# Performance work log

Measured on AMD Instinct MI355X. Metric: run time of the kernel, lower is better.

## Reference

```python
import jax, jax.numpy as jnp
import numpy as np

NPOINT, RADIUS, NSAMPLE = 1024, 0.2, 32


def _fps(xyz, npoint):
    # xyz: (B, N, 3) -> (B, npoint) int32, iterative furthest point sampling
    B, N, _ = xyz.shape

    def step(carry, _):
        dists, far = carry  # (B,N), (B,)
        centroid = jnp.take_along_axis(xyz, far[:, None, None], axis=1)  # (B,1,3)
        d = jnp.sum((xyz - centroid) ** 2, axis=-1)  # (B,N)
        dists = jnp.minimum(dists, d)
        nxt = jnp.argmax(dists, axis=-1).astype(jnp.int32)
        return (dists, nxt), far

    init = (jnp.full((B, N), 1e10, xyz.dtype), jnp.zeros((B,), jnp.int32))
    _, idx = jax.lax.scan(step, init, None, length=npoint)
    return jnp.transpose(idx)  # (B, npoint)


def _ball_query(radius, nsample, xyz, new_xyz):
    # xyz: (B,N,3), new_xyz: (B,S,3) -> (B,S,nsample) int32
    N = xyz.shape[1]
    d2 = jnp.sum((new_xyz[:, :, None, :] - xyz[:, None, :, :]) ** 2, axis=-1)  # (B,S,N)
    # first-nsample-in-range semantics of PointNet++ ball_query
    key = jnp.where(d2 < radius * radius, jnp.arange(N, dtype=jnp.int32), N)
    neg, order = jax.lax.top_k(-key, nsample)  # smallest keys first
    valid = (-neg) < N
    return jnp.where(valid, order, order[..., :1])  # pad with first valid idx


def _group(feat, idx):
    # feat: (B,D,N), idx: (B,S,ns) -> (B,D,S,ns)
    return jax.vmap(lambda f, i: f[:, i])(feat, idx)


def _conv(x, w, b):
    # 1x1 Conv2d: x (B,C,S,ns), w (O,C), b (O)
    return jnp.einsum('oc,bcps->bops', w, x) + b[None, :, None, None]


def _bn(x, s, t):
    # inference BatchNorm folded into per-channel affine
    return x * s[None, :, None, None] + t[None, :, None, None]


def setup_inputs() -> dict:
    key = jax.random.key(0)
    ks = jax.random.split(key, 40)
    B, N, D = 16, 8192, 64
    BCH = 8  # max(8, 64 // 8)

    def w(k, shape, scale=0.1):
        return jax.random.normal(k, shape, jnp.float32) * scale

    def bn(k, c):
        k1, k2 = jax.random.split(k)
        return (jax.random.uniform(k1, (c,), jnp.float32, 0.75, 1.25),
                0.1 * jax.random.normal(k2, (c,), jnp.float32))

    attn_s0, attn_t0 = bn(ks[2], BCH)
    attn_s1, attn_t1 = bn(ks[3], D)
    attn_s2, attn_t2 = bn(ks[4], D)
    mlp_s0, mlp_t0 = bn(ks[5], 64)
    mlp_s1, mlp_t1 = bn(ks[6], 64)
    eca_s, eca_t = bn(ks[7], 128)
    return {
        'xyz': jax.random.uniform(ks[0], (B, 3, N), jnp.float32),
        'points': jax.random.normal(ks[1], (B, D, N), jnp.float32),
        'attn_w0': w(ks[10], (BCH, 3)), 'attn_b0': w(ks[11], (BCH,)),
        'attn_s0': attn_s0, 'attn_t0': attn_t0,
        'attn_w1': w(ks[12], (D, BCH)), 'attn_b1': w(ks[13], (D,)),
        'attn_s1': attn_s1, 'attn_t1': attn_t1,
        'attn_w2': w(ks[14], (D, D)), 'attn_b2': w(ks[15], (D,)),
        'attn_s2': attn_s2, 'attn_t2': attn_t2,
        'mlp_w0': w(ks[16], (64, D)), 'mlp_b0': w(ks[17], (64,)),
        'mlp_s0': mlp_s0, 'mlp_t0': mlp_t0,
        'mlp_w1': w(ks[18], (64, 64)), 'mlp_b1': w(ks[19], (64,)),
        'mlp_s1': mlp_s1, 'mlp_t1': mlp_t1,
        'eca_k': w(ks[20], (3,), 0.5),
        'eca_w': w(ks[21], (128, 64)), 'eca_b': w(ks[22], (128,)),
        'eca_s': eca_s, 'eca_t': eca_t,
    }


def reference(xyz, points,
              attn_w0, attn_b0, attn_s0, attn_t0,
              attn_w1, attn_b1, attn_s1, attn_t1,
              attn_w2, attn_b2, attn_s2, attn_t2,
              mlp_w0, mlp_b0, mlp_s0, mlp_t0,
              mlp_w1, mlp_b1, mlp_s1, mlp_t1,
              eca_k, eca_w, eca_b, eca_s, eca_t):
    xyz_f = jnp.transpose(xyz, (0, 2, 1))  # (B,N,3)
    # 1. sampling + grouping
    fps_idx = _fps(xyz_f, NPOINT)  # (B,S)
    new_xyz = jax.vmap(lambda p, i: p[:, i])(xyz, fps_idx)  # (B,3,S)
    idx = _ball_query(RADIUS, NSAMPLE, xyz_f, jnp.transpose(new_xyz, (0, 2, 1)))
    grouped_xyz = _group(xyz, idx) - new_xyz[..., None]  # (B,3,S,ns)
    x = _group(points, idx)  # (B,D,S,ns)
    # 2. position-attention module
    pos = jax.nn.relu(_bn(_conv(grouped_xyz, attn_w0, attn_b0), attn_s0, attn_t0))
    pos = _bn(_conv(pos, attn_w1, attn_b1), attn_s1, attn_t1)
    x = x + pos
    x = _bn(_conv(x, attn_w2, attn_b2), attn_s2, attn_t2)
    # 3. shared MLP (conv-bn-relu over mlp[:-1])
    x = jax.nn.relu(_bn(_conv(x, mlp_w0, mlp_b0), mlp_s0, mlp_t0))
    x = jax.nn.relu(_bn(_conv(x, mlp_w1, mlp_b1), mlp_s1, mlp_t1))
    # 4. ECA channel attention + final 1x1 conv-bn
    y = jnp.mean(x, axis=(2, 3))  # (B,C)
    yp = jnp.pad(y, ((0, 0), (1, 1)))
    y = eca_k[0] * yp[:, :-2] + eca_k[1] * yp[:, 1:-1] + eca_k[2] * yp[:, 2:]
    x = x * jax.nn.sigmoid(y)[:, :, None, None]
    x = _bn(_conv(x, eca_w, eca_b), eca_s, eca_t)
    # 5. max-pool over neighborhood
    new_features = jnp.max(x, axis=-1)  # (B,128,S)
    return (new_xyz, new_features)
```

## Files before the change

kernel.cpp:

```cpp
#include <hip/hip_runtime.h>

typedef unsigned int   u32;
typedef unsigned long long u64;
typedef float pkf2 __attribute__((ext_vector_type(2)));

#define B_  16
#define N_  8192
#define S_  1024
#define NS_ 32
#define XS_ 68
#define NWORK_ 240
#define NCHUNK_ 4096
#define NFIN_ 512

__device__ __forceinline__ float nanguard(float v) {
  u32 x = __float_as_uint(v);
  if ((x & 0x7F80u) == 0x7F80u) x ^= 0x0080u;
  return __uint_as_float(x);
}

__device__ __forceinline__ float wave_max_nonneg(float v) {
  int x = __float_as_int(v);
#define DPP_STEP(ctrl) \
  x = __float_as_int(fmaxf(__int_as_float(x), \
      __int_as_float(__builtin_amdgcn_update_dpp(0, x, (ctrl), 0xf, 0xf, true))))
  DPP_STEP(0x111);
  DPP_STEP(0x112);
  DPP_STEP(0x114);
  DPP_STEP(0x118);
  DPP_STEP(0x142);
  DPP_STEP(0x143);
#undef DPP_STEP
  return __int_as_float(__builtin_amdgcn_readlane(x, 63));
}

__global__ __launch_bounds__(256) void k_xyzt(const float* __restrict__ xyz, float4* __restrict__ xyzt,
                                              u32* __restrict__ prog) {
  if (blockIdx.x == 0 && blockIdx.y == 0 && threadIdx.x < 16) prog[threadIdx.x] = 0u;
  int b = blockIdx.y;
  int i = blockIdx.x * 256 + threadIdx.x;
  const float* p = xyz + (size_t)b * 3 * N_;
  xyzt[(size_t)b * N_ + i] = make_float4(p[i], p[N_ + i], p[2 * N_ + i], 0.f);
}

__global__ __launch_bounds__(256) void k_ptst(const float* __restrict__ pts, float* __restrict__ ptst) {
  __shared__ float tile[64][65];
  int b = blockIdx.y, n0 = blockIdx.x * 64, t = threadIdx.x;
  {
    int c = t >> 2, j0 = (t & 3) * 16;
    const float4* src = (const float4*)(pts + (size_t)b * 64 * N_ + (size_t)c * N_ + n0 + j0);
#pragma unroll
    for (int q = 0; q < 4; ++q) {
      float4 a = src[q];
      tile[c][j0 + 4*q + 0] = a.x; tile[c][j0 + 4*q + 1] = a.y;
      tile[c][j0 + 4*q + 2] = a.z; tile[c][j0 + 4*q + 3] = a.w;
    }
  }
  __syncthreads();
  {
    int n = t >> 2, c0 = (t & 3) * 16;
    float4* dv = (float4*)(ptst + ((size_t)b * N_ + n0 + n) * 64 + c0);
#pragma unroll
    for (int q = 0; q < 4; ++q)
      dv[q] = make_float4(tile[c0 + 4*q + 0][n], tile[c0 + 4*q + 1][n],
                          tile[c0 + 4*q + 2][n], tile[c0 + 4*q + 3][n]);
  }
}

__global__ __launch_bounds__(1024)
__attribute__((amdgpu_waves_per_eu(4, 4)))
void k_fps(const float4* __restrict__ xyzt,
           float4* __restrict__ nxf,
           float* __restrict__ out_xyz) {
#pragma clang fp contract(off)
  __shared__ float4 ldsp[N_];
  __shared__ u64 slot[4];
  __shared__ int win_hist[S_];
  int b = blockIdx.x, t = threadIdx.x;
  const float4* p4 = xyzt + (size_t)b * N_;
  const float4* pp8 = p4 + t * 8;

  float4 q0 = pp8[0], q1 = pp8[1], q2 = pp8[2], q3 = pp8[3];
  float4 q4 = pp8[4], q5 = pp8[5], q6 = pp8[6], q7 = pp8[7];
  ldsp[t * 8 + 0] = q0; ldsp[t * 8 + 1] = q1; ldsp[t * 8 + 2] = q2; ldsp[t * 8 + 3] = q3;
  ldsp[t * 8 + 4] = q4; ldsp[t * 8 + 5] = q5; ldsp[t * 8 + 6] = q6; ldsp[t * 8 + 7] = q7;

#define DECLPAIR(P, A, B) \
  pkf2 px##P = {q##A.x, q##B.x}; pkf2 py##P = {q##A.y, q##B.y}; \
  pkf2 pz##P = {q##A.z, q##B.z}; pkf2 dm##P = {1e10f, 1e10f};
  DECLPAIR(01, 0, 1) DECLPAIR(23, 2, 3) DECLPAIR(45, 4, 5) DECLPAIR(67, 6, 7)
#undef DECLPAIR
#define PIN(P) asm volatile("" : "+v"(px##P), "+v"(py##P), "+v"(pz##P));
  PIN(01) PIN(23) PIN(45) PIN(67)
#undef PIN

  if (t == 0) {
    slot[0] = 8191ull;
    slot[1] = 0; slot[2] = 0; slot[3] = 0;
    win_hist[0] = 0;
  }
  __syncthreads();
  int lane = t & 63;
  for (int it = 1; it < S_; ++it) {
    u64 w = slot[(it - 1) & 3];
    int widx = 8191 - (int)(w & 0xFFFFFFFFull);
    if (t == 0) { win_hist[it - 1] = widx; slot[(it + 1) & 3] = 0; }
    float4 c = ldsp[widx & (N_ - 1)];
    pkf2 cx2 = {c.x, c.x}, cy2 = {c.y, c.y}, cz2 = {c.z, c.z};
#define UPDP(P) { \
    pkf2 dx = px##P - cx2; pkf2 dy = py##P - cy2; pkf2 dz = pz##P - cz2; \
    pkf2 xx = dx * dx; pkf2 yy = dy * dy; pkf2 zz = dz * dz; \
    pkf2 ss = xx + yy; pkf2 dd = ss + zz; \
    dm##P.x = fminf(dm##P.x, dd.x); dm##P.y = fminf(dm##P.y, dd.y); }
    UPDP(01) UPDP(23) UPDP(45) UPDP(67)
#undef UPDP
    float e0 = dm01.x, e1 = dm01.y, e2 = dm23.x, e3 = dm23.y;
    float e4 = dm45.x, e5 = dm45.y, e6 = dm67.x, e7 = dm67.y;
    float va0 = e1 > e0 ? e1 : e0; int ia0 = e1 > e0 ? 1 : 0;
    float va1 = e3 > e2 ? e3 : e2; int ia1 = e3 > e2 ? 3 : 2;
    float va2 = e5 > e4 ? e5 : e4; int ia2 = e5 > e4 ? 5 : 4;
    float va3 = e7 > e6 ? e7 : e6; int ia3 = e7 > e6 ? 7 : 6;
    float vb0 = va1 > va0 ? va1 : va0; int ib0 = va1 > va0 ? ia1 : ia0;
    float vb1 = va3 > va2 ? va3 : va2; int ib1 = va3 > va2 ? ia3 : ia2;
    float bv = vb1 > vb0 ? vb1 : vb0;  int bk = vb1 > vb0 ? ib1 : ib0;
    int bi = t * 8 + bk;
    float wm = wave_max_nonneg(bv);
    u64 msk = __ballot(bv == wm);
    int wl = __ffsll((long long)msk) - 1;
    int wbi = __builtin_amdgcn_readlane(bi, wl);
    if (lane == 0)
      atomicMax(&slot[it & 3],
                ((u64)__float_as_uint(wm) << 32) | (u64)(u32)(8191 - wbi));
    __syncthreads();
  }
  if (t == 0)
    win_hist[S_ - 1] = 8191 - (int)(slot[(S_ - 1) & 3] & 0xFFFFFFFFull);
  __syncthreads();
  {
    int wi = win_hist[t] & (N_ - 1);
    float4 c = ldsp[wi];
    nxf[(size_t)b * S_ + t] = c;
    float* o = out_xyz + (size_t)b * 3 * S_;
    o[t] = nanguard(c.x); o[S_ + t] = nanguard(c.y); o[2 * S_ + t] = nanguard(c.z);
  }
}

__global__ __launch_bounds__(256) void k_ball(const float4* __restrict__ xyzt,
                                              const float4* __restrict__ nxf,
                                              int* __restrict__ ballidx) {
  int gw = blockIdx.x * 4 + (threadIdx.x >> 6);
  int lane = threadIdx.x & 63;
  int b = gw >> 10, s = gw & 1023;
  float4 c = nxf[(size_t)b * S_ + s];
  const float4* pts = xyzt + (size_t)b * N_;
  int* out = ballidx + (size_t)gw * NS_;
  int cnt = 0, first = 0;
  bool havefirst = false;
  for (int chunk = 0; chunk < N_; chunk += 64) {
    float4 p = pts[chunk + lane];
    float dx = p.x - c.x, dy = p.y - c.y, dz = p.z - c.z;
    float d2 = __fadd_rn(__fadd_rn(__fmul_rn(dx, dx), __fmul_rn(dy, dy)), __fmul_rn(dz, dz));
    bool v = d2 <= 0.04f;
    u64 m = __ballot(v);
    if (m) {
      int pos = cnt + __popcll(m & ((1ull << lane) - 1ull));
      if (v && pos < NS_) out[pos] = chunk + lane;
      if (!havefirst) { first = chunk + (__ffsll((long long)m) - 1); havefirst = true; }
      cnt += __popcll(m);
      if (cnt >= NS_) break;
    }
  }
  if (cnt < NS_) {
    for (int p = cnt + lane; p < NS_; p += 64) out[p] = first;
  }
}

struct ChainSm {
  float Wbuf[64 * XS_];
  float W1f[64 * 9];
  float W0f[8 * 4];
  float s2f[64], sm0f[64], sm1f[64];
  float bb0[8];
  float bb1[64], bb2[64], bm0[64], bm1[64];
  float X[32 * XS_];
  float H[32 * XS_];
  float scratch[384];
  int   idx_s[NS_];
};

__device__ __forceinline__ void stage_w64(float* Wbuf, const float* w, int t) {
  int c = t >> 2, q = (t & 3) * 16;
  const float4* src = (const float4*)(w + c * 64 + q);
  float4* dst = (float4*)(Wbuf + c * XS_ + q);
  dst[0] = src[0]; dst[1] = src[1]; dst[2] = src[2]; dst[3] = src[3];
}

template<bool RELU>
__device__ __forceinline__ void gemm64(const float* __restrict__ Wbuf,
                                       const float* __restrict__ Xin,
                                       float* __restrict__ Yout,
                                       const float* __restrict__ scl,
                                       const float* __restrict__ bia,
                                       int lane, int n0) {
  float acc[8] = {0,0,0,0,0,0,0,0};
#pragma unroll
  for (int k4 = 0; k4 < 16; ++k4) {
    float4 wq = *(const float4*)&Wbuf[lane * XS_ + k4 * 4];
#pragma unroll
    for (int nj = 0; nj < 8; ++nj) {
      float4 xq = *(const float4*)&Xin[(n0 + nj) * XS_ + k4 * 4];
      acc[nj] += wq.x * xq.x; acc[nj] += wq.y * xq.y;
      acc[nj] += wq.z * xq.z; acc[nj] += wq.w * xq.w;
    }
  }
  float sc = scl[lane], bi = bia[lane];
#pragma unroll
  for (int nj = 0; nj < 8; ++nj) {
    float v = sc * acc[nj] + bi;
    Yout[(n0 + nj) * XS_ + lane] = RELU ? fmaxf(v, 0.f) : v;
  }
}

template<bool USE_PTST>
__device__ __forceinline__ void chain_tile(ChainSm& sm, int b, int s, int bs,
    const float4* xyzt, const float* ptst, const float* points,
    const float4* nxf, const int* ballidx,
    const float* w0, const float* b0, const float* s0, const float* t0,
    const float* w1, const float* b1, const float* s1, const float* t1,
    const float* w2, const float* b2, const float* s2, const float* t2,
    const float* m0w, const float* m0b, const float* m0s, const float* m0t,
    const float* m1w, const float* m1b, const float* m1s, const float* m1t) {
  int t = threadIdx.x, lane = t & 63, g = t >> 6, n0 = g * 8;

  stage_w64(sm.Wbuf, w2, t);
  if (t < 64) {
    float v2 = s2[t];  sm.s2f[t] = v2;  sm.bb2[t] = v2 * b2[t] + t2[t];
    float vm0 = m0s[t]; sm.sm0f[t] = vm0; sm.bm0[t] = vm0 * m0b[t] + m0t[t];
    float vm1 = m1s[t]; sm.sm1f[t] = vm1; sm.bm1[t] = vm1 * m1b[t] + m1t[t];
    float v1 = s1[t];
#pragma unroll
    for (int k = 0; k < 8; ++k) sm.W1f[t * 9 + k] = v1 * w1[t * 8 + k];
    sm.bb1[t] = v1 * b1[t] + t1[t];
  }
  if (t < 8) {
    float v0 = s0[t];
#pragma unroll
    for (int k = 0; k < 3; ++k) sm.W0f[t * 4 + k] = v0 * w0[t * 3 + k];
    sm.bb0[t] = v0 * b0[t] + t0[t];
  }
  if (t < NS_) sm.idx_s[t] = ballidx[(size_t)bs * NS_ + t] & (N_ - 1);
  __syncthreads();

  {
    int n = t >> 3, c8 = (t & 7) * 8;
    int pi = sm.idx_s[n];
    if (USE_PTST) {
      const float4* v = (const float4*)(ptst + ((size_t)b * N_ + pi) * 64 + c8);
      float4* xr = (float4*)&sm.X[n * XS_ + c8];
      xr[0] = v[0]; xr[1] = v[1];
    } else {
      const float* pp = points + (size_t)b * 64 * N_ + (size_t)c8 * N_ + pi;
#pragma unroll
      for (int j = 0; j < 8; ++j) sm.X[n * XS_ + c8 + j] = pp[(size_t)j * N_];
    }
  }
  if (t < NS_) {
    float4 p = xyzt[(size_t)b * N_ + sm.idx_s[t]];
    float4 cc = nxf[(size_t)b * S_ + s];
    float* gx = &sm.scratch[256 + t * 4];
    gx[0] = p.x - cc.x; gx[1] = p.y - cc.y; gx[2] = p.z - cc.z;
  }
  __syncthreads();

  {
    int n = t >> 3, cc = t & 7;
    const float* gx = &sm.scratch[256 + n * 4];
    float a = sm.bb0[cc];
    a += sm.W0f[cc * 4 + 0] * gx[0];
    a += sm.W0f[cc * 4 + 1] * gx[1];
    a += sm.W0f[cc * 4 + 2] * gx[2];
    sm.scratch[n * 8 + cc] = fmaxf(a, 0.f);
  }
  {
#pragma unroll
    for (int nj = 0; nj < 8; ++nj) {
      float a = sm.bb1[lane];
      const float* p8 = &sm.scratch[(n0 + nj) * 8];
#pragma unroll
      for (int k = 0; k < 8; ++k) a += sm.W1f[lane * 9 + k] * p8[k];
      sm.X[(n0 + nj) * XS_ + lane] += a;
    }
  }
  gemm64<false>(sm.Wbuf, sm.X, sm.H, sm.s2f, sm.bb2, lane, n0);
  __syncthreads();
  stage_w64(sm.Wbuf, m0w, t);
  __syncthreads();
  gemm64<true>(sm.Wbuf, sm.H, sm.X, sm.sm0f, sm.bm0, lane, n0);
  __syncthreads();
  stage_w64(sm.Wbuf, m1w, t);
  __syncthreads();
  gemm64<true>(sm.Wbuf, sm.X, sm.H, sm.sm1f, sm.bm1, lane, n0);
}

template<bool USE_PTST, bool WRITE_H2>
__global__ __launch_bounds__(256) void k_chain(
    const float4* __restrict__ xyzt, const float* __restrict__ ptst,
    const float* __restrict__ points,
    const float4* __restrict__ nxf, const int* __restrict__ ballidx,
    const float* w0, const float* b0, const float* s0, const float* t0,
    const float* w1, const float* b1, const float* s1, const float* t1,
    const float* w2, const float* b2, const float* s2, const float* t2,
    const float* m0w, const float* m0b, const float* m0s, const float* m0t,
    const float* m1w, const float* m1b, const float* m1s, const float* m1t,
    float* __restrict__ h2out, float* __restrict__ partials) {
  __shared__ ChainSm sm;
  int t = threadIdx.x, bs = blockIdx.x;
  int b = bs >> 10, s = bs & 1023;
  int lane = t & 63, g = t >> 6, n0 = g * 8;

  chain_tile<USE_PTST>(sm, b, s, bs, xyzt, ptst, points, nxf, ballidx,
                       w0, b0, s0, t0, w1, b1, s1, t1, w2, b2, s2, t2,
                       m0w, m0b, m0s, m0t, m1w, m1b, m1s, m1t);

  float* psum = sm.scratch;
  float lsum = 0.f;
#pragma unroll
  for (int nj = 0; nj < 8; ++nj) {
    float r = sm.H[(n0 + nj) * XS_ + lane];
    lsum += r;
    if (WRITE_H2)
      h2out[((size_t)bs * 32 + n0 + nj) * 64 + lane] = r;
  }
  psum[lane * 5 + g] = lsum;
  __syncthreads();
  if (t < 64) {
    float v = (psum[t * 5 + 0] + psum[t * 5 + 1]) + (psum[t * 5 + 2] + psum[t * 5 + 3]);
    partials[(size_t)bs * 64 + t] = v;
  }
}

struct ChainSub {
  float X[32 * XS_];
  float H[32 * XS_];
  float scratch[384];
  int   idx_s[NS_];
};
struct WkSm {
  float Wc2[64 * XS_];
  float Wm0[64 * XS_];
  float Wm1[64 * XS_];
  float W1f[64 * 9];
  float W0f[8 * 4];
  float s2f[64], sm0f[64], sm1f[64];
  float bb0[8];
  float bb1[64], bb2[64], bm0[64], bm1[64];
  ChainSub sub[4];
};
struct FpsSm {
  float4 ldsp[N_];
  u64 slot[4];
  int win_hist[S_];
};
union FusedSm { FpsSm f; WkSm w; };
static_assert(sizeof(FusedSm) <= 160 * 1024, "LDS overflow");

__global__ __launch_bounds__(1024)
__attribute__((amdgpu_waves_per_eu(4, 4)))
void k_fused(const float4* __restrict__ xyzt, const float* __restrict__ ptst,
             float4* __restrict__ nxf, float* __restrict__ out_xyz,
             u32* __restrict__ prog,
             const float* w0, const float* b0, const float* s0, const float* t0,
             const float* w1, const float* b1, const float* s1, const float* t1,
             const float* w2, const float* b2, const float* s2, const float* t2,
             const float* m0w, const float* m0b, const float* m0s, const float* m0t,
             const float* m1w, const float* m1b, const float* m1s, const float* m1t,
             float* __restrict__ h2out, float* __restrict__ partials) {
  __shared__ FusedSm smu;
  int t = threadIdx.x;

  if (blockIdx.x < B_) {
#pragma clang fp contract(off)
    FpsSm& fs = smu.f;
    int b = blockIdx.x;
    const float4* p4 = xyzt + (size_t)b * N_;
    const float4* pp8 = p4 + t * 8;

    float4 q0 = pp8[0], q1 = pp8[1], q2 = pp8[2], q3 = pp8[3];
    float4 q4 = pp8[4], q5 = pp8[5], q6 = pp8[6], q7 = pp8[7];
    fs.ldsp[t * 8 + 0] = q0; fs.ldsp[t * 8 + 1] = q1; fs.ldsp[t * 8 + 2] = q2; fs.ldsp[t * 8 + 3] = q3;
    fs.ldsp[t * 8 + 4] = q4; fs.ldsp[t * 8 + 5] = q5; fs.ldsp[t * 8 + 6] = q6; fs.ldsp[t * 8 + 7] = q7;

#define DECLPAIR(P, A, B) \
    pkf2 px##P = {q##A.x, q##B.x}; pkf2 py##P = {q##A.y, q##B.y}; \
    pkf2 pz##P = {q##A.z, q##B.z}; pkf2 dm##P = {1e10f, 1e10f};
    DECLPAIR(01, 0, 1) DECLPAIR(23, 2, 3) DECLPAIR(45, 4, 5) DECLPAIR(67, 6, 7)
#undef DECLPAIR
#define PIN(P) asm volatile("" : "+v"(px##P), "+v"(py##P), "+v"(pz##P));
    PIN(01) PIN(23) PIN(45) PIN(67)
#undef PIN

    if (t == 0) {
      fs.slot[0] = 8191ull;
      fs.slot[1] = 0; fs.slot[2] = 0; fs.slot[3] = 0;
      fs.win_hist[0] = 0;
    }
    __syncthreads();
    int lane = t & 63;
    for (int it = 1; it < S_; ++it) {
      u64 w = fs.slot[(it - 1) & 3];
      int widx = 8191 - (int)(w & 0xFFFFFFFFull);
      float4 c = fs.ldsp[widx & (N_ - 1)];
      if (t == 0) {
        fs.win_hist[it - 1] = widx; fs.slot[(it + 1) & 3] = 0;
        if ((it & 15) == 0)
          __hip_atomic_store(&prog[b], (u32)(it - 1), __ATOMIC_RELEASE, __HIP_MEMORY_SCOPE_AGENT);
        nxf[(size_t)b * S_ + (it - 1)] = c;
      }
      pkf2 cx2 = {c.x, c.x}, cy2 = {c.y, c.y}, cz2 = {c.z, c.z};
#define UPDP(P) { \
      pkf2 dx = px##P - cx2; pkf2 dy = py##P - cy2; pkf2 dz = pz##P - cz2; \
      pkf2 xx = dx * dx; pkf2 yy = dy * dy; pkf2 zz = dz * dz; \
      pkf2 ss = xx + yy; pkf2 dd = ss + zz; \
      dm##P.x = fminf(dm##P.x, dd.x); dm##P.y = fminf(dm##P.y, dd.y); }
      UPDP(01) UPDP(23) UPDP(45) UPDP(67)
#undef UPDP
      float e0 = dm01.x, e1 = dm01.y, e2 = dm23.x, e3 = dm23.y;
      float e4 = dm45.x, e5 = dm45.y, e6 = dm67.x, e7 = dm67.y;
      float va0 = e1 > e0 ? e1 : e0; int ia0 = e1 > e0 ? 1 : 0;
      float va1 = e3 > e2 ? e3 : e2; int ia1 = e3 > e2 ? 3 : 2;
      float va2 = e5 > e4 ? e5 : e4; int ia2 = e5 > e4 ? 5 : 4;
      float va3 = e7 > e6 ? e7 : e6; int ia3 = e7 > e6 ? 7 : 6;
      float vb0 = va1 > va0 ? va1 : va0; int ib0 = va1 > va0 ? ia1 : ia0;
      float vb1 = va3 > va2 ? va3 : va2; int ib1 = va3 > va2 ? ia3 : ia2;
      float bv = vb1 > vb0 ? vb1 : vb0;  int bk = vb1 > vb0 ? ib1 : ib0;
      int bi = t * 8 + bk;
      float wm = wave_max_nonneg(bv);
      u64 msk = __ballot(bv == wm);
      int wl = __ffsll((long long)msk) - 1;
      int wbi = __builtin_amdgcn_readlane(bi, wl);
      if (lane == 0)
        atomicMax(&fs.slot[it & 3],
                  ((u64)__float_as_uint(wm) << 32) | (u64)(u32)(8191 - wbi));
      __syncthreads();
    }
    if (t == 0) {
      int wl_ = 8191 - (int)(fs.slot[(S_ - 1) & 3] & 0xFFFFFFFFull);
      fs.win_hist[S_ - 1] = wl_;
      float4 c = fs.ldsp[wl_ & (N_ - 1)];
      nxf[(size_t)b * S_ + (S_ - 1)] = c;
    }
    __syncthreads();
    {
      int wi = fs.win_hist[t] & (N_ - 1);
      float4 c = fs.ldsp[wi];
      float* o = out_xyz + (size_t)b * 3 * S_;
      o[t] = nanguard(c.x); o[S_ + t] = nanguard(c.y); o[2 * S_ + t] = nanguard(c.z);
    }
    if (t == 0)
      __hip_atomic_store(&prog[b], (u32)S_, __ATOMIC_RELEASE, __HIP_MEMORY_SCOPE_AGENT);
    return;
  }

  WkSm& wk = smu.w;
  int w = blockIdx.x - B_;
  if (t < 256) {
    stage_w64(wk.Wc2, w2, t);
    stage_w64(wk.Wm0, m0w, t);
    stage_w64(wk.Wm1, m1w, t);
  }
  if (t < 64) {
    float v2 = s2[t];  wk.s2f[t] = v2;  wk.bb2[t] = v2 * b2[t] + t2[t];
    float vm0 = m0s[t]; wk.sm0f[t] = vm0; wk.bm0[t] = vm0 * m0b[t] + m0t[t];
    float vm1 = m1s[t]; wk.sm1f[t] = vm1; wk.bm1[t] = vm1 * m1b[t] + m1t[t];
    float v1 = s1[t];
#pragma unroll
    for (int k = 0; k < 8; ++k) wk.W1f[t * 9 + k] = v1 * w1[t * 8 + k];
    wk.bb1[t] = v1 * b1[t] + t1[t];
  }
  if (t < 8) {
    float v0 = s0[t];
#pragma unroll
    for (int k = 0; k < 3; ++k) wk.W0f[t * 4 + k] = v0 * w0[t * 3 + k];
    wk.bb0[t] = v0 * b0[t] + t0[t];
  }
  __syncthreads();

  int sg = t >> 8, tid = t & 255, lane = t & 63, g2 = (t >> 6) & 3, n0 = g2 * 8;
  ChainSub& cs = wk.sub[sg];

  for (int ck = w; ck < NCHUNK_; ck += NWORK_) {
    int s = ck >> 2, bg = ck & 3, b = bg * 4 + sg;
    if (t == 0) {
      int bbase = bg * 4;
#pragma unroll
      for (int j = 0; j < 4; ++j) {
        while (__hip_atomic_load(&prog[bbase + j], __ATOMIC_RELAXED, __HIP_MEMORY_SCOPE_AGENT) < (u32)(s + 1))
          __builtin_amdgcn_s_sleep(32);
      }
      (void)__hip_atomic_load(&prog[bbase], __ATOMIC_ACQUIRE, __HIP_MEMORY_SCOPE_AGENT);
    }
    __syncthreads();

    float4 cc;
    if (g2 == 0) {
      cc = nxf[(size_t)b * S_ + s];
      const float4* pts = xyzt + (size_t)b * N_;
      int cnt = 0, first = 0;
      bool havefirst = false;
      for (int chunk = 0; chunk < N_; chunk += 64) {
        float4 p = pts[chunk + lane];
        float dx = p.x - cc.x, dy = p.y - cc.y, dz = p.z - cc.z;
        float d2 = __fadd_rn(__fadd_rn(__fmul_rn(dx, dx), __fmul_rn(dy, dy)), __fmul_rn(dz, dz));
        bool v = d2 <= 0.04f;
        u64 m = __ballot(v);
        if (m) {
          int pos = cnt + __popcll(m & ((1ull << lane) - 1ull));
          if (v && pos < NS_) cs.idx_s[pos] = chunk + lane;
          if (!havefirst) { first = chunk + (__ffsll((long long)m) - 1); havefirst = true; }
          cnt += __popcll(m);
          if (cnt >= NS_) break;
        }
      }
      if (cnt < NS_) {
        for (int p = cnt + lane; p < NS_; p += 64) cs.idx_s[p] = first;
      }
    }
    __syncthreads();

    {
      int n = tid >> 3, c8 = (tid & 7) * 8;
      int pi = cs.idx_s[n];
      const float4* v = (const float4*)(ptst + ((size_t)b * N_ + pi) * 64 + c8);
      float4* xr = (float4*)&cs.X[n * XS_ + c8];
      xr[0] = v[0]; xr[1] = v[1];
    }
    if (tid < NS_) {
      float4 p = xyzt[(size_t)b * N_ + cs.idx_s[tid]];
      float* gx = &cs.scratch[256 + tid * 4];
      gx[0] = p.x - cc.x; gx[1] = p.y - cc.y; gx[2] = p.z - cc.z;
    }
    __syncthreads();

    {
      int n = tid >> 3, ch = tid & 7;
      const float* gx = &cs.scratch[256 + n * 4];
      float a = wk.bb0[ch];
      a += wk.W0f[ch * 4 + 0] * gx[0];
      a += wk.W0f[ch * 4 + 1] * gx[1];
      a += wk.W0f[ch * 4 + 2] * gx[2];
      cs.scratch[n * 8 + ch] = fmaxf(a, 0.f);
    }
    {
#pragma unroll
      for (int nj = 0; nj < 8; ++nj) {
        float a = wk.bb1[lane];
        const float* p8 = &cs.scratch[(n0 + nj) * 8];
#pragma unroll
        for (int k = 0; k < 8; ++k) a += wk.W1f[lane * 9 + k] * p8[k];
        cs.X[(n0 + nj) * XS_ + lane] += a;
      }
    }
    gemm64<false>(wk.Wc2, cs.X, cs.H, wk.s2f, wk.bb2, lane, n0);
    gemm64<true >(wk.Wm0, cs.H, cs.X, wk.sm0f, wk.bm0, lane, n0);
    gemm64<true >(wk.Wm1, cs.X, cs.H, wk.sm1f, wk.bm1, lane, n0);

    int bs = (b << 10) | s;
    float lsum = 0.f;
#pragma unroll
    for (int nj = 0; nj < 8; ++nj) {
      float r = cs.H[(n0 + nj) * XS_ + lane];
      lsum += r;
      h2out[((size_t)bs * 32 + n0 + nj) * 64 + lane] = r;
    }
    __syncthreads();
    cs.scratch[lane * 5 + g2] = lsum;
    __syncthreads();
    if (tid < 64) {
      float v = (cs.scratch[tid * 5 + 0] + cs.scratch[tid * 5 + 1]) +
                (cs.scratch[tid * 5 + 2] + cs.scratch[tid * 5 + 3]);
      partials[(size_t)bs * 64 + tid] = v;
    }
  }
}

__global__ __launch_bounds__(256) void k_eca(const float* __restrict__ partials,
                                             const float* __restrict__ ecak,
                                             float* __restrict__ sig) {
  __shared__ float red[64 * 5];
  __shared__ float yy[66];
  int b = blockIdx.x, t = threadIdx.x;
  int c = t & 63, sg = t >> 6;
  float acc = 0.f;
  for (int s = sg; s < S_; s += 4) acc += partials[((size_t)b * S_ + s) * 64 + c];
  red[c * 5 + sg] = acc;
  __syncthreads();
  if (t < 64) {
    float v = (red[t * 5 + 0] + red[t * 5 + 1]) + (red[t * 5 + 2] + red[t * 5 + 3]);
    yy[t + 1] = v * (1.f / 32768.f);
  }
  if (t == 64) { yy[0] = 0.f; yy[65] = 0.f; }
  __syncthreads();
  if (t < 64) {
    float gv = ecak[0] * yy[t] + ecak[1] * yy[t + 1] + ecak[2] * yy[t + 2];
    sig[b * 64 + t] = 1.f / (1.f + expf(-gv));
  }
}

__global__ __launch_bounds__(256, 2) void k_final_h2(const float* __restrict__ h2,
                                                     const float* __restrict__ sig,
                                                     const float* ew, const float* eb,
                                                     const float* es, const float* et,
                                                     float* __restrict__ outf) {
  __shared__ float Wh[128 * XS_];
  __shared__ float esf[128], bbf[128];
  __shared__ float X2[4][32 * XS_];
  int t = threadIdx.x;
  {
    int c2 = t >> 1, h = (t & 1) * 32;
    const float4* src = (const float4*)(ew + c2 * 64 + h);
    float4* dst = (float4*)(Wh + c2 * XS_ + h);
#pragma unroll
    for (int j = 0; j < 8; ++j) dst[j] = src[j];
  }
  if (t < 128) { float v = es[t]; esf[t] = v; bbf[t] = v * eb[t] + et[t]; }
  __syncthreads();

  int wv = t >> 6, lane = t & 63;
  int cg = lane & 15, rg = lane >> 4;
  float* X = X2[wv];
  int gw = blockIdx.x * 4 + wv;

  for (int bs = gw; bs < B_ * S_; bs += NFIN_ * 4) {
    int b = bs >> 10, s = bs & 1023;
    {
      float4 sgl = *(const float4*)&sig[b * 64 + cg * 4];
      const float4* hsrc = (const float4*)(h2 + (size_t)bs * 2048);
#pragma unroll
      for (int m = 0; m < 8; ++m) {
        int q = lane + 64 * m;
        float4 v = hsrc[q];
        v.x *= sgl.x; v.y *= sgl.y; v.z *= sgl.z; v.w *= sgl.w;
        *(float4*)&X[(q >> 4) * XS_ + (q & 15) * 4] = v;
      }
    }
#pragma unroll
    for (int half = 0; half < 2; ++half) {
      float acc[4][8];
#pragma unroll
      for (int i = 0; i < 4; ++i)
#pragma unroll
        for (int j = 0; j < 8; ++j) acc[i][j] = 0.f;
#pragma unroll
      for (int k4 = 0; k4 < 16; ++k4) {
        float4 xq[8];
#pragma unroll
        for (int j = 0; j < 8; ++j)
          xq[j] = *(const float4*)&X[(rg + 4 * j) * XS_ + k4 * 4];
#pragma unroll
        for (int i = 0; i < 4; ++i) {
          float4 wq = *(const float4*)&Wh[(half * 64 + cg + 16 * i) * XS_ + k4 * 4];
#pragma unroll
          for (int j = 0; j < 8; ++j) {
            acc[i][j] += wq.x * xq[j].x; acc[i][j] += wq.y * xq[j].y;
            acc[i][j] += wq.z * xq[j].z; acc[i][j] += wq.w * xq[j].w;
          }
        }
      }
      float m0, m1, m2, m3;
#define RED(i, mv) { \
      float a0 = fmaxf(fmaxf(acc[i][0], acc[i][1]), fmaxf(acc[i][2], acc[i][3])); \
      float a1 = fmaxf(fmaxf(acc[i][4], acc[i][5]), fmaxf(acc[i][6], acc[i][7])); \
      mv = fmaxf(a0, a1); \
      mv = fmaxf(mv, __shfl_xor(mv, 16)); \
      mv = fmaxf(mv, __shfl_xor(mv, 32)); }
      RED(0, m0) RED(1, m1) RED(2, m2) RED(3, m3)
#undef RED
      float msel = rg == 0 ? m0 : rg == 1 ? m1 : rg == 2 ? m2 : m3;
      int c = half * 64 + cg + 16 * rg;
      outf[((size_t)b * 128 + c) * S_ + s] = nanguard(esf[c] * msel + bbf[c]);
    }
  }
}

__device__ __forceinline__ void final_gemm(const float* __restrict__ WA,
                                           const float* __restrict__ WB,
                                           const float* __restrict__ X2,
                                           const float* __restrict__ esf,
                                           const float* __restrict__ bbf,
                                           float* __restrict__ zred,
                                           float* __restrict__ outf,
                                           int b, int s, int t) {
  int lane = t & 63, g = t >> 6, n0 = g * 8;
  float aA[8] = {0,0,0,0,0,0,0,0}, aB[8] = {0,0,0,0,0,0,0,0};
#pragma unroll
  for (int k4 = 0; k4 < 16; ++k4) {
    float4 wqA = *(const float4*)&WA[lane * XS_ + k4 * 4];
    float4 wqB = *(const float4*)&WB[lane * XS_ + k4 * 4];
#pragma unroll
    for (int nj = 0; nj < 8; ++nj) {
      float4 xq = *(const float4*)&X2[(n0 + nj) * XS_ + k4 * 4];
      aA[nj] += wqA.x * xq.x; aA[nj] += wqA.y * xq.y;
      aA[nj] += wqA.z * xq.z; aA[nj] += wqA.w * xq.w;
      aB[nj] += wqB.x * xq.x; aB[nj] += wqB.y * xq.y;
      aB[nj] += wqB.z * xq.z; aB[nj] += wqB.w * xq.w;
    }
  }
  float mA = aA[0], mB = aB[0];
#pragma unroll
  for (int j = 1; j < 8; ++j) { mA = fmaxf(mA, aA[j]); mB = fmaxf(mB, aB[j]); }
  zred[lane * 5 + g]        = esf[lane] * mA + bbf[lane];
  zred[(lane + 64) * 5 + g] = esf[lane + 64] * mB + bbf[lane + 64];
  __syncthreads();
  if (t < 128) {
    float m = fmaxf(fmaxf(zred[t * 5 + 0], zred[t * 5 + 1]),
                    fmaxf(zred[t * 5 + 2], zred[t * 5 + 3]));
    outf[((size_t)b * 128 + t) * S_ + s] = nanguard(m);
  }
}

template<bool USE_PTST>
__global__ __launch_bounds__(256) void k_final_rec(
    const float4* __restrict__ xyzt, const float* __restrict__ ptst,
    const float* __restrict__ points,
    const float4* __restrict__ nxf, const int* __restrict__ ballidx,
    const float* w0, const float* b0, const float* s0, const float* t0,
    const float* w1, const float* b1, const float* s1, const float* t1,
    const float* w2, const float* b2, const float* s2, const float* t2,
    const float* m0w, const float* m0b, const float* m0s, const float* m0t,
    const float* m1w, const float* m1b, const float* m1s, const float* m1t,
    const float* __restrict__ sig,
    const float* ew, const float* eb, const float* es, const float* et,
    float* __restrict__ outf) {
  __shared__ ChainSm sm;
  __shared__ float Wb2[64 * XS_];
  __shared__ float esf2[128], bbf2[128], sigl2[64];
  __shared__ float zred[128 * 5];
  int t = threadIdx.x, bs = blockIdx.x;
  int b = bs >> 10, s = bs & 1023;
  int lane = t & 63, g = t >> 6, n0 = g * 8;

  chain_tile<USE_PTST>(sm, b, s, bs, xyzt, ptst, points, nxf, ballidx,
                       w0, b0, s0, t0, w1, b1, s1, t1, w2, b2, s2, t2,
                       m0w, m0b, m0s, m0t, m1w, m1b, m1s, m1t);

  __syncthreads();
  stage_w64(sm.Wbuf, ew, t);
  stage_w64(Wb2, ew + 64 * 64, t);
  if (t < 128) {
    float v = es[t]; esf2[t] = v; bbf2[t] = v * eb[t] + et[t];
  }
  if (t < 64) sigl2[t] = sig[b * 64 + t];
  __syncthreads();
  {
#pragma unroll
    for (int nj = 0; nj < 8; ++nj)
      sm.X[(n0 + nj) * XS_ + lane] = sigl2[lane] * sm.H[(n0 + nj) * XS_ + lane];
  }
  final_gemm(sm.Wbuf, Wb2, sm.X, esf2, bbf2, zred, outf, b, s, t);
}

extern "C" void kernel_launch(void* const* d_in, const int* in_sizes, int n_in,
                              void* d_out, int out_size, void* d_ws, size_t ws_size,
                              hipStream_t stream) {
  const float* xyz    = (const float*)d_in[0];
  const float* points = (const float*)d_in[1];
  const float* w0 = (const float*)d_in[2],  *b0 = (const float*)d_in[3],  *s0 = (const float*)d_in[4],  *t0 = (const float*)d_in[5];
  const float* w1 = (const float*)d_in[6],  *b1 = (const float*)d_in[7],  *s1 = (const float*)d_in[8],  *t1 = (const float*)d_in[9];
  const float* w2 = (const float*)d_in[10], *b2 = (const float*)d_in[11], *s2 = (const float*)d_in[12], *t2 = (const float*)d_in[13];
  const float* m0w = (const float*)d_in[14], *m0b = (const float*)d_in[15], *m0s = (const float*)d_in[16], *m0t = (const float*)d_in[17];
  const float* m1w = (const float*)d_in[18], *m1b = (const float*)d_in[19], *m1s = (const float*)d_in[20], *m1t = (const float*)d_in[21];
  const float* ecak = (const float*)d_in[22];
  const float* ew = (const float*)d_in[23], *eb = (const float*)d_in[24], *es = (const float*)d_in[25], *et = (const float*)d_in[26];

  const size_t OFF_XYZT = 0;
  const size_t OFF_NXF  = 2097152;
  const size_t OFF_BIDX = 2359296;
  const size_t OFF_PART = 4456448;
  const size_t OFF_SIG  = 8650752;
  const size_t OFF_PTST = 8654848;
  const size_t OFF_H2   = 42209280;
  const size_t NEED_PTST = OFF_H2;
  const size_t NEED_H2   = 176427008;

  const bool use_ptst = ws_size >= NEED_PTST;
  const bool use_h2   = ws_size >= NEED_H2;

  char* ws = (char*)d_ws;
  float4* xyzt    = (float4*)(ws + OFF_XYZT);
  float4* nxf     = (float4*)(ws + OFF_NXF);
  int*    ballidx = (int*)   (ws + OFF_BIDX);
  u32*    prog    = (u32*)   (ws + OFF_BIDX);
  float*  partials= (float*) (ws + OFF_PART);
  float*  sig     = (float*) (ws + OFF_SIG);
  float*  ptst    = (float*) (ws + OFF_PTST);
  float*  h2      = (float*) (ws + OFF_H2);

  float* out_xyz  = (float*)d_out;
  float* out_feat = (float*)d_out + (size_t)B_ * 3 * S_;

  k_xyzt<<<dim3(N_ / 256, B_), 256, 0, stream>>>(xyz, xyzt, prog);
  if (use_ptst)
    k_ptst<<<dim3(N_ / 64, B_), 256, 0, stream>>>(points, ptst);

  if (use_h2) {
    k_fused<<<B_ + NWORK_, 1024, 0, stream>>>(xyzt, ptst, nxf, out_xyz, prog,
        w0, b0, s0, t0, w1, b1, s1, t1, w2, b2, s2, t2,
        m0w, m0b, m0s, m0t, m1w, m1b, m1s, m1t, h2, partials);
    k_eca<<<B_, 256, 0, stream>>>(partials, ecak, sig);
    k_final_h2<<<NFIN_, 256, 0, stream>>>(h2, sig, ew, eb, es, et, out_feat);
  } else if (use_ptst) {
    k_fps <<<B_, 1024, 0, stream>>>(xyzt, nxf, out_xyz);
    k_ball<<<(B_ * S_) / 4, 256, 0, stream>>>(xyzt, nxf, ballidx);
    k_chain<true, false><<<B_ * S_, 256, 0, stream>>>(xyzt, ptst, points, nxf, ballidx,
        w0, b0, s0, t0, w1, b1, s1, t1, w2, b2, s2, t2,
        m0w, m0b, m0s, m0t, m1w, m1b, m1s, m1t, h2, partials);
    k_eca<<<B_, 256, 0, stream>>>(partials, ecak, sig);
    k_final_rec<true><<<B_ * S_, 256, 0, stream>>>(xyzt, ptst, points, nxf, ballidx,
        w0, b0, s0, t0, w1, b1, s1, t1, w2, b2, s2, t2,
        m0w, m0b, m0s, m0t, m1w, m1b, m1s, m1t, sig, ew, eb, es, et, out_feat);
  } else {
    k_fps <<<B_, 1024, 0, stream>>>(xyzt, nxf, out_xyz);
    k_ball<<<(B_ * S_) / 4, 256, 0, stream>>>(xyzt, nxf, ballidx);
    k_chain<false, false><<<B_ * S_, 256, 0, stream>>>(xyzt, ptst, points, nxf, ballidx,
        w0, b0, s0, t0, w1, b1, s1, t1, w2, b2, s2, t2,
        m0w, m0b, m0s, m0t, m1w, m1b, m1s, m1t, h2, partials);
    k_eca<<<B_, 256, 0, stream>>>(partials, ecak, sig);
    k_final_rec<false><<<B_ * S_, 256, 0, stream>>>(xyzt, ptst, points, nxf, ballidx,
        w0, b0, s0, t0, w1, b1, s1, t1, w2, b2, s2, t2,
        m0w, m0b, m0s, m0t, m1w, m1b, m1s, m1t, sig, ew, eb, es, et, out_feat);
  }
}
```

Measured before the change: 1.245 ms.

## Fold ECA and final conv into fused persistent kernel via grid-wide counters

Removes the separate ECA and final conv/max-pool launches by running both inside the persistent fused kernel. Global atomic counters act as grid barriers: the FPS blocks wait for all worker blocks, compute the per-batch sigmoid gate, then signal, and every block then runs its slice of the final GEMM and max-pool. The final phase now reads h2 straight from global memory instead of staging it in LDS. This saves launch gaps and the tail of earlier stages, but relies on all 256 blocks being co-resident (spin-wait deadlock risk otherwise) and replaces LDS reuse with uncached-looking global loads.

```diff
diff --git a/kernel.cpp b/kernel.cpp
--- a/kernel.cpp
+++ b/kernel.cpp
@@ -11,7 +11,6 @@
 #define XS_ 68
 #define NWORK_ 240
 #define NCHUNK_ 4096
-#define NFIN_ 512
 
 __device__ __forceinline__ float nanguard(float v) {
   u32 x = __float_as_uint(v);
@@ -36,7 +35,7 @@
 
 __global__ __launch_bounds__(256) void k_xyzt(const float* __restrict__ xyz, float4* __restrict__ xyzt,
                                               u32* __restrict__ prog) {
-  if (blockIdx.x == 0 && blockIdx.y == 0 && threadIdx.x < 16) prog[threadIdx.x] = 0u;
+  if (blockIdx.x == 0 && blockIdx.y == 0 && threadIdx.x < 18) prog[threadIdx.x] = 0u;
   int b = blockIdx.y;
   int i = blockIdx.x * 256 + threadIdx.x;
   const float* p = xyz + (size_t)b * 3 * N_;
@@ -361,8 +360,87 @@
   u64 slot[4];
   int win_hist[S_];
 };
-union FusedSm { FpsSm f; WkSm w; };
+struct FinSm {
+  float Wh[128 * XS_];
+  float esf[128], bbf[128];
+  float sigl[64];
+  float red[64 * 5];
+  float yy[66];
+};
+union FusedSm { FpsSm f; WkSm w; FinSm fin; };
 static_assert(sizeof(FusedSm) <= 160 * 1024, "LDS overflow");
+
+__device__ __forceinline__ void final_phase(FinSm& fin, int t, int blkid, u32* prog,
+    const float* __restrict__ h2, const float* __restrict__ sig,
+    const float* __restrict__ ew, const float* __restrict__ es,
+    const float* __restrict__ eb, const float* __restrict__ et,
+    float* __restrict__ outf) {
+  if (t < 256) {
+    int c2 = t >> 1, h = (t & 1) * 32;
+    const float4* src = (const float4*)(ew + c2 * 64 + h);
+    float4* dst = (float4*)(fin.Wh + c2 * XS_ + h);
+#pragma unroll
+    for (int j = 0; j < 8; ++j) dst[j] = src[j];
+  }
+  if (t < 128) { float v = es[t]; fin.esf[t] = v; fin.bbf[t] = v * eb[t] + et[t]; }
+  if (t == 0) {
+    while (__hip_atomic_load(&prog[17], __ATOMIC_RELAXED, __HIP_MEMORY_SCOPE_AGENT) < 16u)
+      __builtin_amdgcn_s_sleep(8);
+    (void)__hip_atomic_load(&prog[17], __ATOMIC_ACQUIRE, __HIP_MEMORY_SCOPE_AGENT);
+  }
+  __syncthreads();
+  if (t < 64) fin.sigl[t] = sig[(blkid >> 4) * 64 + t];
+  __syncthreads();
+
+  int wv = t >> 6, lane = t & 63;
+  int cg = lane & 15, rg = lane >> 4;
+#pragma unroll
+  for (int it = 0; it < 4; ++it) {
+    int bs = blkid * 64 + it * 16 + wv;
+    int b = bs >> 10, s = bs & 1023;
+    const float* hsrc = h2 + (size_t)bs * 2048;
+#pragma unroll
+    for (int half = 0; half < 2; ++half) {
+      float acc[4][8];
+#pragma unroll
+      for (int i = 0; i < 4; ++i)
+#pragma unroll
+        for (int j = 0; j < 8; ++j) acc[i][j] = 0.f;
+#pragma unroll
+      for (int k4 = 0; k4 < 16; ++k4) {
+        float4 sgl = *(const float4*)&fin.sigl[k4 * 4];
+        float4 xq[8];
+#pragma unroll
+        for (int j = 0; j < 8; ++j) {
+          float4 v = *(const float4*)&hsrc[(size_t)(rg + 4 * j) * 64 + k4 * 4];
+          v.x *= sgl.x; v.y *= sgl.y; v.z *= sgl.z; v.w *= sgl.w;
+          xq[j] = v;
+        }
+#pragma unroll
+        for (int i = 0; i < 4; ++i) {
+          float4 wq = *(const float4*)&fin.Wh[(half * 64 + cg + 16 * i) * XS_ + k4 * 4];
+#pragma unroll
+          for (int j = 0; j < 8; ++j) {
+            acc[i][j] += wq.x * xq[j].x; acc[i][j] += wq.y * xq[j].y;
+            acc[i][j] += wq.z * xq[j].z; acc[i][j] += wq.w * xq[j].w;
+          }
+        }
+      }
+      float m0, m1, m2, m3;
+#define RED(i, mv) { \
+      float a0 = fmaxf(fmaxf(acc[i][0], acc[i][1]), fmaxf(acc[i][2], acc[i][3])); \
+      float a1 = fmaxf(fmaxf(acc[i][4], acc[i][5]), fmaxf(acc[i][6], acc[i][7])); \
+      mv = fmaxf(a0, a1); \
+      mv = fmaxf(mv, __shfl_xor(mv, 16)); \
+      mv = fmaxf(mv, __shfl_xor(mv, 32)); }
+      RED(0, m0) RED(1, m1) RED(2, m2) RED(3, m3)
+#undef RED
+      float msel = rg == 0 ? m0 : rg == 1 ? m1 : rg == 2 ? m2 : m3;
+      int c = half * 64 + cg + 16 * rg;
+      outf[((size_t)b * 128 + c) * S_ + s] = nanguard(fin.esf[c] * msel + fin.bbf[c]);
+    }
+  }
+}
 
 __global__ __launch_bounds__(1024)
 __attribute__((amdgpu_waves_per_eu(4, 4)))
@@ -374,7 +452,11 @@
              const float* w2, const float* b2, const float* s2, const float* t2,
              const float* m0w, const float* m0b, const float* m0s, const float* m0t,
              const float* m1w, const float* m1b, const float* m1s, const float* m1t,
-             float* __restrict__ h2out, float* __restrict__ partials) {
+             float* __restrict__ h2out, float* __restrict__ partials,
+             const float* __restrict__ ecak,
+             const float* __restrict__ ew, const float* __restrict__ eb,
+             const float* __restrict__ es, const float* __restrict__ et,
+             float* __restrict__ sig, float* __restrict__ outf) {
   __shared__ FusedSm smu;
   int t = threadIdx.x;
 
@@ -458,6 +540,38 @@
     }
     if (t == 0)
       __hip_atomic_store(&prog[b], (u32)S_, __ATOMIC_RELEASE, __HIP_MEMORY_SCOPE_AGENT);
+
+    __syncthreads();
+    FinSm& fin = smu.fin;
+    if (t == 0) {
+      while (__hip_atomic_load(&prog[16], __ATOMIC_RELAXED, __HIP_MEMORY_SCOPE_AGENT) < (u32)NWORK_)
+        __builtin_amdgcn_s_sleep(32);
+      (void)__hip_atomic_load(&prog[16], __ATOMIC_ACQUIRE, __HIP_MEMORY_SCOPE_AGENT);
+    }
+    __syncthreads();
+    if (t < 256) {
+      int c = t & 63, sg = t >> 6;
+      float acc = 0.f;
+      for (int s2 = sg; s2 < S_; s2 += 4)
+        acc += partials[((size_t)b * S_ + s2) * 64 + c];
+      fin.red[c * 5 + sg] = acc;
+    }
+    __syncthreads();
+    if (t < 64) {
+      float v = (fin.red[t * 5 + 0] + fin.red[t * 5 + 1]) + (fin.red[t * 5 + 2] + fin.red[t * 5 + 3]);
+      fin.yy[t + 1] = v * (1.f / 32768.f);
+    }
+    if (t == 64) { fin.yy[0] = 0.f; fin.yy[65] = 0.f; }
+    __syncthreads();
+    if (t < 64) {
+      float gv = ecak[0] * fin.yy[t] + ecak[1] * fin.yy[t + 1] + ecak[2] * fin.yy[t + 2];
+      sig[b * 64 + t] = 1.f / (1.f + expf(-gv));
+    }
+    __threadfence();
+    __syncthreads();
+    if (t == 0)
+      __hip_atomic_fetch_add(&prog[17], 1u, __ATOMIC_RELEASE, __HIP_MEMORY_SCOPE_AGENT);
+    final_phase(fin, t, blockIdx.x, prog, h2out, sig, ew, es, eb, et, outf);
     return;
   }
 
@@ -581,6 +695,12 @@
       partials[(size_t)bs * 64 + tid] = v;
     }
   }
+
+  __threadfence();
+  __syncthreads();
+  if (t == 0)
+    __hip_atomic_fetch_add(&prog[16], 1u, __ATOMIC_RELEASE, __HIP_MEMORY_SCOPE_AGENT);
+  final_phase(smu.fin, t, blockIdx.x, prog, h2out, sig, ew, es, eb, et, outf);
 }
 
 __global__ __launch_bounds__(256) void k_eca(const float* __restrict__ partials,
@@ -603,82 +723,6 @@
   if (t < 64) {
     float gv = ecak[0] * yy[t] + ecak[1] * yy[t + 1] + ecak[2] * yy[t + 2];
     sig[b * 64 + t] = 1.f / (1.f + expf(-gv));
-  }
-}
-
-__global__ __launch_bounds__(256, 2) void k_final_h2(const float* __restrict__ h2,
-                                                     const float* __restrict__ sig,
-                                                     const float* ew, const float* eb,
-                                                     const float* es, const float* et,
-                                                     float* __restrict__ outf) {
-  __shared__ float Wh[128 * XS_];
-  __shared__ float esf[128], bbf[128];
-  __shared__ float X2[4][32 * XS_];
-  int t = threadIdx.x;
-  {
-    int c2 = t >> 1, h = (t & 1) * 32;
-    const float4* src = (const float4*)(ew + c2 * 64 + h);
-    float4* dst = (float4*)(Wh + c2 * XS_ + h);
-#pragma unroll
-    for (int j = 0; j < 8; ++j) dst[j] = src[j];
-  }
-  if (t < 128) { float v = es[t]; esf[t] = v; bbf[t] = v * eb[t] + et[t]; }
-  __syncthreads();
-
-  int wv = t >> 6, lane = t & 63;
-  int cg = lane & 15, rg = lane >> 4;
-  float* X = X2[wv];
-  int gw = blockIdx.x * 4 + wv;
-
-  for (int bs = gw; bs < B_ * S_; bs += NFIN_ * 4) {
-    int b = bs >> 10, s = bs & 1023;
-    {
-      float4 sgl = *(const float4*)&sig[b * 64 + cg * 4];
-      const float4* hsrc = (const float4*)(h2 + (size_t)bs * 2048);
-#pragma unroll
-      for (int m = 0; m < 8; ++m) {
-        int q = lane + 64 * m;
-        float4 v = hsrc[q];
-        v.x *= sgl.x; v.y *= sgl.y; v.z *= sgl.z; v.w *= sgl.w;
-        *(float4*)&X[(q >> 4) * XS_ + (q & 15) * 4] = v;
-      }
-    }
-#pragma unroll
-    for (int half = 0; half < 2; ++half) {
-      float acc[4][8];
-#pragma unroll
-      for (int i = 0; i < 4; ++i)
-#pragma unroll
-        for (int j = 0; j < 8; ++j) acc[i][j] = 0.f;
-#pragma unroll
-      for (int k4 = 0; k4 < 16; ++k4) {
-        float4 xq[8];
-#pragma unroll
-        for (int j = 0; j < 8; ++j)
-          xq[j] = *(const float4*)&X[(rg + 4 * j) * XS_ + k4 * 4];
-#pragma unroll
-        for (int i = 0; i < 4; ++i) {
-          float4 wq = *(const float4*)&Wh[(half * 64 + cg + 16 * i) * XS_ + k4 * 4];
-#pragma unroll
-          for (int j = 0; j < 8; ++j) {
-            acc[i][j] += wq.x * xq[j].x; acc[i][j] += wq.y * xq[j].y;
-            acc[i][j] += wq.z * xq[j].z; acc[i][j] += wq.w * xq[j].w;
-          }
-        }
-      }
-      float m0, m1, m2, m3;
-#define RED(i, mv) { \
-      float a0 = fmaxf(fmaxf(acc[i][0], acc[i][1]), fmaxf(acc[i][2], acc[i][3])); \
-      float a1 = fmaxf(fmaxf(acc[i][4], acc[i][5]), fmaxf(acc[i][6], acc[i][7])); \
-      mv = fmaxf(a0, a1); \
-      mv = fmaxf(mv, __shfl_xor(mv, 16)); \
-      mv = fmaxf(mv, __shfl_xor(mv, 32)); }
-      RED(0, m0) RED(1, m1) RED(2, m2) RED(3, m3)
-#undef RED
-      float msel = rg == 0 ? m0 : rg == 1 ? m1 : rg == 2 ? m2 : m3;
-      int c = half * 64 + cg + 16 * rg;
-      outf[((size_t)b * 128 + c) * S_ + s] = nanguard(esf[c] * msel + bbf[c]);
-    }
   }
 }
 
@@ -805,9 +849,8 @@
   if (use_h2) {
     k_fused<<<B_ + NWORK_, 1024, 0, stream>>>(xyzt, ptst, nxf, out_xyz, prog,
         w0, b0, s0, t0, w1, b1, s1, t1, w2, b2, s2, t2,
-        m0w, m0b, m0s, m0t, m1w, m1b, m1s, m1t, h2, partials);
-    k_eca<<<B_, 256, 0, stream>>>(partials, ecak, sig);
-    k_final_h2<<<NFIN_, 256, 0, stream>>>(h2, sig, ew, eb, es, et, out_feat);
+        m0w, m0b, m0s, m0t, m1w, m1b, m1s, m1t, h2, partials,
+        ecak, ew, eb, es, et, sig, out_feat);
   } else if (use_ptst) {
     k_fps <<<B_, 1024, 0, stream>>>(xyzt, nxf, out_xyz);
     k_ball<<<(B_ * S_) / 4, 256, 0, stream>>>(xyzt, nxf, ballidx);
```

Result: slower. 2.255 ms (+81.0%).
